# Kernel optimization log

Measured on AMD Instinct MI355X. Metric: run time of the kernel, lower is better.

## Reference

```python
import jax, jax.numpy as jnp
import numpy as np

B, S, D_IN, D_OUT = 4, 4096, 256, 256

def setup_inputs() -> dict:
    key = jax.random.key(0)
    ks = jax.random.split(key, 7)
    scale = 1.0 / np.sqrt(D_IN)
    return {
        "x": jax.random.normal(ks[0], (B, S, D_IN), dtype=jnp.float32),
        "Wq": jax.random.uniform(ks[1], (D_IN, D_OUT), jnp.float32, -scale, scale),
        "bq": jax.random.uniform(ks[2], (D_OUT,), jnp.float32, -scale, scale),
        "Wk": jax.random.uniform(ks[3], (D_IN, D_OUT), jnp.float32, -scale, scale),
        "bk": jax.random.uniform(ks[4], (D_OUT,), jnp.float32, -scale, scale),
        "Wv": jax.random.uniform(ks[5], (D_IN, D_OUT), jnp.float32, -scale, scale),
        "bv": jax.random.uniform(ks[6], (D_OUT,), jnp.float32, -scale, scale),
    }

def reference(x, Wq, bq, Wk, bk, Wv, bv):
    # QKV projections: [B, S, D_OUT]
    q = jnp.einsum("bsd,de->bse", x, Wq) + bq
    k = jnp.einsum("bsd,de->bse", x, Wk) + bk
    v = jnp.einsum("bsd,de->bse", x, Wv) + bv
    # Scaled dot-product attention; full [B, S, S] scores as in the original.
    scores = jnp.einsum("bqe,bke->bqk", q, k) / jnp.sqrt(jnp.asarray(q.shape[-1], q.dtype))
    attn = jax.nn.softmax(scores, axis=-1)
    return jnp.einsum("bqk,bke->bqe", attn, v)
```

## Files before the change

### kernel.cpp

```cpp
#include <hip/hip_runtime.h>
#include <stdint.h>

typedef unsigned short u16;
typedef long long i64;
typedef __attribute__((ext_vector_type(4))) float f32x4;
typedef __attribute__((ext_vector_type(8))) short bf16x8;
typedef __attribute__((ext_vector_type(4))) int i32x4;
typedef __attribute__((ext_vector_type(2))) unsigned int u32x2;

#define SEQ 4096
#define DIM 256
#define QS4 0.36067376f

__device__ __forceinline__ u16 f2bf(float f) {
  union { float f; uint32_t u; } v; v.f = f;
  uint32_t r = (v.u + 0x7FFFu + ((v.u >> 16) & 1u)) >> 16;
  return (u16)r;
}

__device__ __forceinline__ float bf2f(u16 u) {
  union { uint32_t u; float f; } v; v.u = ((uint32_t)u) << 16;
  return v.f;
}

__device__ __forceinline__ uint8_t f2fp8(float f) {
  return (uint8_t)__builtin_amdgcn_cvt_pk_fp8_f32(f, 0.f, 0, false);
}

__device__ __forceinline__ void gload_lds16(const void* g, void* lds) {
  __builtin_amdgcn_global_load_lds(
      (const __attribute__((address_space(1))) uint32_t*)g,
      (__attribute__((address_space(3))) uint32_t*)lds, 16, 0, 0);
}

__device__ __forceinline__ f32x4 mfma8(i64 a, i64 b, f32x4 c) {
  return __builtin_amdgcn_mfma_f32_16x16x32_fp8_fp8(a, b, c, 0, 0, 0);
}

__global__ __launch_bounds__(256) void wt_kernel(const float* __restrict__ Wq,
                                                 const float* __restrict__ Wk,
                                                 const float* __restrict__ Wv,
                                                 u16* __restrict__ wt) {
  int b = blockIdx.x;
  int w = b >> 8;
  int n = b & 255;
  const float* W = (w == 0) ? Wq : ((w == 1) ? Wk : Wv);
  float scale = (w == 0) ? QS4 : ((w == 1) ? 0.25f : 1.0f);
  int k = threadIdx.x;
  wt[(w * 256 + n) * 256 + k] = f2bf(W[k * 256 + n] * scale);
}

__global__ __launch_bounds__(256) void qkv_kernel(
    const float* __restrict__ x, const float* __restrict__ bq,
    const float* __restrict__ bk, const float* __restrict__ bv,
    const u16* __restrict__ wt, uint8_t* __restrict__ qs,
    uint8_t* __restrict__ kk, char* __restrict__ vt) {
  __shared__ __align__(16) char lds_b[65536];
  __shared__ __align__(16) u16 lds_v[4096];
  int tid = threadIdx.x;
  int w = tid >> 6, l = tid & 63;
  int a = l & 15, g = l >> 4;
  int rowbase = blockIdx.x * 64;

  uint32_t wso[8];
#pragma unroll
  for (int j = 0; j < 8; ++j) {
    uint32_t inst = w * 8 + j;
    uint32_t flat = inst * 1024 + l * 16;
    uint32_t row = flat >> 9;
    uint32_t c5 = (flat >> 4) & 31;
    uint32_t sc = (c5 & ~7u) | ((c5 ^ row) & 7u);
    wso[j] = row * 512 + sc * 16;
  }
  uint32_t bro[8];
#pragma unroll
  for (int ks = 0; ks < 8; ++ks) {
    uint32_t c5 = ks * 4 + g;
    uint32_t sc = (c5 & ~7u) | ((c5 ^ (a & 7u)) & 7u);
    bro[ks] = (uint32_t)a * 512 + sc * 16;
  }

  bf16x8 afr[8];
  {
    int row = rowbase + w * 16 + a;
    const f32x4* xr4 = (const f32x4*)(x + (size_t)row * 256);
#pragma unroll
    for (int ks = 0; ks < 8; ++ks) {
      int q4 = ks * 8 + g * 2;
      f32x4 lo = xr4[q4], hi = xr4[q4 + 1];
      union { bf16x8 s; u16 u[8]; } fr;
      fr.u[0] = f2bf(lo[0]); fr.u[1] = f2bf(lo[1]);
      fr.u[2] = f2bf(lo[2]); fr.u[3] = f2bf(lo[3]);
      fr.u[4] = f2bf(hi[0]); fr.u[5] = f2bf(hi[1]);
      fr.u[6] = f2bf(hi[2]); fr.u[7] = f2bf(hi[3]);
      afr[ks] = fr.s;
    }
  }

#pragma unroll
  for (int j = 0; j < 8; ++j)
    gload_lds16((const char*)wt + wso[j], lds_b + (w * 8 + j) * 1024);

  int cur = 0;
  for (int it = 0; it < 12; ++it) {
    asm volatile("s_waitcnt vmcnt(0) lgkmcnt(0)" ::: "memory");
    __builtin_amdgcn_s_barrier();
    __builtin_amdgcn_sched_barrier(0);
    if (it < 11) {
#pragma unroll
      for (int j = 0; j < 8; ++j)
        gload_lds16((const char*)wt + (size_t)(it + 1) * 32768 + wso[j],
                    lds_b + (cur ^ 1) * 32768 + (w * 8 + j) * 1024);
    }
    int w3 = it >> 2, qn = it & 3;
    f32x4 acc[4];
#pragma unroll
    for (int n0 = 0; n0 < 4; ++n0) acc[n0] = (f32x4){0.f, 0.f, 0.f, 0.f};
#pragma unroll
    for (int ks = 0; ks < 8; ++ks) {
#pragma unroll
      for (int n0 = 0; n0 < 4; ++n0) {
        bf16x8 bfr = *(const bf16x8*)(lds_b + cur * 32768 + bro[ks] + n0 * 8192);
        acc[n0] = __builtin_amdgcn_mfma_f32_16x16x32_bf16(afr[ks], bfr, acc[n0], 0, 0, 0);
      }
    }
    const float* bias = (w3 == 0) ? bq : ((w3 == 1) ? bk : bv);
    if (w3 < 2) {
      uint8_t* out8 = (w3 == 0) ? qs : kk;
      float bscale = (w3 == 0) ? QS4 : 0.25f;
#pragma unroll
      for (int n0 = 0; n0 < 4; ++n0) {
        int col = qn * 64 + n0 * 16 + a;
        float bb = bias[col] * bscale;
#pragma unroll
        for (int r = 0; r < 4; ++r) {
          int row = rowbase + w * 16 + g * 4 + r;
          out8[(size_t)row * 256 + col] = f2fp8(acc[n0][r] + bb);
        }
      }
    } else {
#pragma unroll
      for (int n0 = 0; n0 < 4; ++n0) {
        int col = qn * 64 + n0 * 16 + a;
        float bb = bias[col];
        int dl = n0 * 16 + a;
#pragma unroll
        for (int r = 0; r < 4; ++r) {
          int m = w * 16 + g * 4 + r;
          uint32_t byteoff =
              (uint32_t)dl * 128 + ((((uint32_t)m >> 3) ^ ((uint32_t)dl & 7)) << 4) + (m & 7) * 2;
          *(u16*)((char*)lds_v + byteoff) = f2bf(acc[n0][r] + bb);
        }
      }
      asm volatile("s_waitcnt lgkmcnt(0)" ::: "memory");
      __builtin_amdgcn_s_barrier();
      {
        int dl = tid >> 2;
        size_t base = (size_t)blockIdx.x * 32768 + (size_t)(qn * 64 + dl) * 128;
#pragma unroll
        for (int cc = 0; cc < 2; ++cc) {
          uint32_t c = (tid & 3) + cc * 4;
          i32x4 vd = *(const i32x4*)((const char*)lds_v + dl * 128 + ((c ^ (dl & 7)) << 4));
          *(i32x4*)(vt + base + c * 16) = vd;
        }
      }
    }
    cur ^= 1;
  }
}

#define VVB 32768u
#define PVB 98304u

#define PV_STEP(SLOT)                                                          \
  {                                                                            \
    bf16x8 pfr[2][2];                                                          \
    _Pragma("unroll") for (int mt = 0; mt < 2; ++mt)                           \
    _Pragma("unroll") for (int j2 = 0; j2 < 2; ++j2)                           \
        pfr[mt][j2] = *(const bf16x8*)(lds + PVB + (SLOT) * 16384 + pro[j2] +  \
                                       mt * 2048);                             \
    __builtin_amdgcn_s_setprio(1);                                             \
    _Pragma("unroll") for (int mt = 0; mt < 2; ++mt)                           \
    _Pragma("unroll") for (int j2 = 0; j2 < 2; ++j2)                           \
        lacc[mt] = __builtin_amdgcn_mfma_f32_16x16x32_bf16(pfr[mt][j2], ones,  \
                                                           lacc[mt], 0, 0, 0); \
    _Pragma("unroll") for (int d0 = 0; d0 < 8; ++d0)                           \
    _Pragma("unroll") for (int j2 = 0; j2 < 2; ++j2) {                         \
      bf16x8 vfr = *(const bf16x8*)(lds + VVB + (SLOT) * 32768 + vro[j2] +     \
                                    d0 * 2048);                                \
      o[0][d0] = __builtin_amdgcn_mfma_f32_16x16x32_bf16(pfr[0][j2], vfr, o[0][d0], 0, 0, 0); \
      o[1][d0] = __builtin_amdgcn_mfma_f32_16x16x32_bf16(pfr[1][j2], vfr, o[1][d0], 0, 0, 0); \
    }                                                                          \
    __builtin_amdgcn_s_setprio(0);                                             \
  }

#define QKEXP(CUR)                                                             \
  {                                                                            \
    f32x4 sc[2][2];                                                            \
    _Pragma("unroll") for (int mt = 0; mt < 2; ++mt)                           \
    _Pragma("unroll") for (int n = 0; n < 2; ++n)                              \
        sc[mt][n] = (f32x4){0.f, 0.f, 0.f, 0.f};                               \
    __builtin_amdgcn_s_setprio(1);                                             \
    _Pragma("unroll") for (int n = 0; n < 2; ++n)                              \
    _Pragma("unroll") for (int j = 0; j < 8; ++j) {                            \
      i64 kfr = *(const i64*)(lds + (CUR) * 16384 + kro[j] + n * 4096);        \
      sc[0][n] = mfma8(kfr, qfr[0][j], sc[0][n]);                              \
      sc[1][n] = mfma8(kfr, qfr[1][j], sc[1][n]);                              \
    }                                                                          \
    __builtin_amdgcn_s_setprio(0);                                             \
    _Pragma("unroll") for (int mt = 0; mt < 2; ++mt)                           \
    _Pragma("unroll") for (int n = 0; n < 2; ++n) {                            \
      float e0 = exp2f(sc[mt][n][0]);                                          \
      float e1 = exp2f(sc[mt][n][1]);                                          \
      float e2 = exp2f(sc[mt][n][2]);                                          \
      float e3 = exp2f(sc[mt][n][3]);                                          \
      uint32_t p0 = (uint32_t)f2bf(e0) | ((uint32_t)f2bf(e1) << 16);           \
      uint32_t p1 = (uint32_t)f2bf(e2) | ((uint32_t)f2bf(e3) << 16);           \
      u32x2 pk = {p0, p1};                                                     \
      *(u32x2*)(lds + PVB + (CUR) * 16384 + pwo[n] + mt * 2048) = pk;          \
    }                                                                          \
  }

#define TILE(CUR, DO_PV, DO_K)                                                 \
  {                                                                            \
    asm volatile("s_waitcnt vmcnt(0) lgkmcnt(0)" ::: "memory");                \
    __builtin_amdgcn_s_barrier();                                              \
    __builtin_amdgcn_sched_barrier(0);                                         \
    _Pragma("unroll") for (int j = 0; j < 4; ++j)                              \
        gload_lds16(vstp + vso[j], lds + VVB + (CUR) * 32768 + (w * 4 + j) * 1024); \
    if (DO_K) {                                                                \
      gload_lds16(kstp + kso[0], lds + ((CUR) ^ 1) * 16384 + (w * 2 + 0) * 1024); \
      gload_lds16(kstp + kso[1], lds + ((CUR) ^ 1) * 16384 + (w * 2 + 1) * 1024); \
    }                                                                          \
    kstp += 16384;                                                             \
    vstp += 32768;                                                             \
    if (w & 1) {                                                               \
      if (DO_PV) PV_STEP((CUR) ^ 1)                                            \
      QKEXP(CUR)                                                               \
    } else {                                                                   \
      QKEXP(CUR)                                                               \
      if (DO_PV) PV_STEP((CUR) ^ 1)                                            \
    }                                                                          \
  }

__global__ __launch_bounds__(512, 1) void attn_kernel(
    const uint8_t* __restrict__ qs, const uint8_t* __restrict__ kk,
    const char* __restrict__ vt, float* __restrict__ out,
    u16* __restrict__ pOB, float* __restrict__ pl, int split) {
  __shared__ __align__(16) char lds[131072];
  int tid = threadIdx.x;
  int w = tid >> 6, l = tid & 63;
  int a = l & 15, g = l >> 4;
  int qq = w >> 1, sub = w & 1;
  int bx = blockIdx.x;
  int h, batch, qt;
  if (split == 2) { h = bx & 1; batch = (bx >> 1) & 3; qt = bx >> 3; }
  else            { h = 0;      batch = (bx >> 1) & 3; qt = ((bx >> 3) << 1) | (bx & 1); }
  int ntHalf = (split == 2) ? 16 : 32;

  uint32_t a7 = a & 7;
  uint32_t kro[8], vro[2], pro[2], pwo[2], kso[2], vso[4];
  {
    uint32_t row = (uint32_t)(sub * 32 + a);
#pragma unroll
    for (int j = 0; j < 8; ++j) {
      uint32_t c4 = j * 2 + (g >> 1);
      kro[j] = row * 256 + (((c4 & ~7u) | ((c4 ^ a7) & 7u)) << 4) + (g & 1) * 8;
    }
  }
#pragma unroll
  for (int j2 = 0; j2 < 2; ++j2)
    vro[j2] = (uint32_t)(sub * 128 + a) * 128 +
              ((((uint32_t)(j2 * 4 + g)) ^ a7) << 4);
  {
    uint32_t q = (uint32_t)(qq * 32 + a);
#pragma unroll
    for (int j2 = 0; j2 < 2; ++j2)
      pro[j2] = q * 128 + ((((uint32_t)(j2 * 4 + g)) ^ a7) << 4);
#pragma unroll
    for (int n = 0; n < 2; ++n)
      pwo[n] = q * 128 +
               ((((uint32_t)(sub * 4 + n * 2 + (g >> 1))) ^ a7) << 4) + (g & 1) * 8;
  }
#pragma unroll
  for (int j = 0; j < 2; ++j) {
    uint32_t inst = w * 2 + j, flat = inst * 1024 + l * 16;
    uint32_t row = flat >> 8, c4 = (flat >> 4) & 15;
    kso[j] = row * 256 + (((c4 & ~7u) | ((c4 ^ (row & 7u)) & 7u)) << 4);
  }
#pragma unroll
  for (int j = 0; j < 4; ++j) {
    uint32_t inst = w * 4 + j, flat = inst * 1024 + l * 16;
    uint32_t row = flat >> 7, c3 = (flat >> 4) & 7;
    vso[j] = row * 128 + ((c3 ^ (row & 7)) << 4);
  }

  i64 qfr[2][8];
  {
    const uint8_t* qp = qs + (size_t)(batch * SEQ + qt * 128) * 256;
#pragma unroll
    for (int mt = 0; mt < 2; ++mt)
#pragma unroll
      for (int j = 0; j < 8; ++j)
        qfr[mt][j] = *(const i64*)(qp + (size_t)(qq * 32 + mt * 16 + a) * 256 +
                                   j * 32 + g * 8);
  }

  f32x4 o[2][8];
  f32x4 lacc[2];
#pragma unroll
  for (int mt = 0; mt < 2; ++mt) {
    lacc[mt] = (f32x4){0.f, 0.f, 0.f, 0.f};
#pragma unroll
    for (int d0 = 0; d0 < 8; ++d0) o[mt][d0] = (f32x4){0.f, 0.f, 0.f, 0.f};
  }
  const short ob = (short)0x3F80;
  bf16x8 ones = {ob, ob, ob, ob, ob, ob, ob, ob};

  const uint8_t* kstp = kk + (size_t)batch * SEQ * 256 + (size_t)h * 2048 * 256;
  const char* vstp = vt + (size_t)batch * 64 * 32768 + (size_t)h * 32 * 32768;

  gload_lds16(kstp + kso[0], lds + (w * 2 + 0) * 1024);
  gload_lds16(kstp + kso[1], lds + (w * 2 + 1) * 1024);
  kstp += 16384;

  TILE(0, false, true)
  for (int tp = 0; tp < ntHalf - 1; ++tp) {
    TILE(1, true, true)
    TILE(0, true, true)
  }
  TILE(1, true, false)

  asm volatile("s_waitcnt vmcnt(0) lgkmcnt(0)" ::: "memory");
  __builtin_amdgcn_s_barrier();
  __builtin_amdgcn_sched_barrier(0);
  PV_STEP(1)

  size_t obase = (size_t)(batch * SEQ + qt * 128 + qq * 32) * 256 + sub * 128;
  if (h == 0) {
#pragma unroll
    for (int mt = 0; mt < 2; ++mt)
#pragma unroll
      for (int r = 0; r < 4; ++r) {
#pragma unroll
        for (int d0 = 0; d0 < 8; ++d0)
          out[obase + (size_t)(mt * 16 + g * 4 + r) * 256 + d0 * 16 + a] = o[mt][d0][r];
      }
  } else {
#pragma unroll
    for (int mt = 0; mt < 2; ++mt)
#pragma unroll
      for (int r = 0; r < 4; ++r) {
#pragma unroll
        for (int d0 = 0; d0 < 8; ++d0)
          pOB[obase + (size_t)(mt * 16 + g * 4 + r) * 256 + d0 * 16 + a] =
              f2bf(o[mt][d0][r]);
      }
  }
  if (a == 0 && sub == 0) {
#pragma unroll
    for (int mt = 0; mt < 2; ++mt)
#pragma unroll
      for (int r = 0; r < 4; ++r)
        pl[h * 16384 + (batch * 32 + qt) * 128 + qq * 32 + mt * 16 + g * 4 + r] =
            lacc[mt][r];
  }
}

__global__ __launch_bounds__(256) void combine_kernel(float* __restrict__ out,
                                                      const u16* __restrict__ pOB,
                                                      const float* __restrict__ pl,
                                                      int split) {
  int b = blockIdx.x;
  int tid = threadIdx.x;
  int batch = b >> 12;
  int rem = b & 4095;
  int qt = rem >> 7, ql = rem & 127;
  size_t idx = (size_t)b * 256 + tid;
  int li = (batch * 32 + qt) * 128 + ql;
  float lA = pl[li];
  float v;
  if (split == 2) {
    float lB = pl[16384 + li];
    v = (out[idx] + bf2f(pOB[idx])) / (lA + lB);
  } else {
    v = out[idx] / lA;
  }
  out[idx] = v;
}

extern "C" void kernel_launch(void* const* d_in, const int* in_sizes, int n_in,
                              void* d_out, int out_size, void* d_ws, size_t ws_size,
                              hipStream_t stream) {
  const float* x = (const float*)d_in[0];
  const float* Wq = (const float*)d_in[1];
  const float* bq = (const float*)d_in[2];
  const float* Wk = (const float*)d_in[3];
  const float* bk = (const float*)d_in[4];
  const float* Wv = (const float*)d_in[5];
  const float* bv = (const float*)d_in[6];
  char* ws = (char*)d_ws;
  u16* wt = (u16*)ws;
  uint8_t* qs = (uint8_t*)(ws + 0x60000);
  uint8_t* kk = (uint8_t*)(ws + 0x460000);
  char* vt = ws + 0x860000;
  float* pl = (float*)(ws + 0x1060000);
  u16* pOB = (u16*)(ws + 0x1080000);
  int split = (ws_size >= 0x1880000ull) ? 2 : 1;
  wt_kernel<<<dim3(768), dim3(256), 0, stream>>>(Wq, Wk, Wv, wt);
  qkv_kernel<<<dim3(256), dim3(256), 0, stream>>>(x, bq, bk, bv, wt, qs, kk, vt);
  attn_kernel<<<dim3(split * 128), dim3(512), 0, stream>>>(qs, kk, vt, (float*)d_out,
                                                           pOB, pl, split);
  combine_kernel<<<dim3(16384), dim3(256), 0, stream>>>((float*)d_out, pOB, pl, split);
}
```

Baseline: 120.8 us.

## Split attention work across 16 waves per block instead of 8

Doubles the workgroup to 1024 threads, so each wave covers 16 key rows for QK and 64 output columns for PV instead of 32 and 128. This halves per-wave accumulator registers and per-wave work, aiming for more latency hiding through extra waves per CU. The alternating QK/PV ordering between wave pairs is dropped in favour of a fixed QK-then-PV order, and each wave issues fewer global-to-LDS loads. The cost is more waves contending at each barrier and a lost staggering of MFMA versus exp phases.

After: 114.1 us. -5.5%, faster.

```diff
diff --git a/kernel.cpp b/kernel.cpp
--- a/kernel.cpp
+++ b/kernel.cpp
@@ -184,7 +184,7 @@
     _Pragma("unroll") for (int j2 = 0; j2 < 2; ++j2)                           \
         lacc[mt] = __builtin_amdgcn_mfma_f32_16x16x32_bf16(pfr[mt][j2], ones,  \
                                                            lacc[mt], 0, 0, 0); \
-    _Pragma("unroll") for (int d0 = 0; d0 < 8; ++d0)                           \
+    _Pragma("unroll") for (int d0 = 0; d0 < 4; ++d0)                           \
     _Pragma("unroll") for (int j2 = 0; j2 < 2; ++j2) {                         \
       bf16x8 vfr = *(const bf16x8*)(lds + VVB + (SLOT) * 32768 + vro[j2] +     \
                                     d0 * 2048);                                \
@@ -194,56 +194,41 @@
     __builtin_amdgcn_s_setprio(0);                                             \
   }
 
-#define QKEXP(CUR)                                                             \
-  {                                                                            \
-    f32x4 sc[2][2];                                                            \
-    _Pragma("unroll") for (int mt = 0; mt < 2; ++mt)                           \
-    _Pragma("unroll") for (int n = 0; n < 2; ++n)                              \
-        sc[mt][n] = (f32x4){0.f, 0.f, 0.f, 0.f};                               \
-    __builtin_amdgcn_s_setprio(1);                                             \
-    _Pragma("unroll") for (int n = 0; n < 2; ++n)                              \
-    _Pragma("unroll") for (int j = 0; j < 8; ++j) {                            \
-      i64 kfr = *(const i64*)(lds + (CUR) * 16384 + kro[j] + n * 4096);        \
-      sc[0][n] = mfma8(kfr, qfr[0][j], sc[0][n]);                              \
-      sc[1][n] = mfma8(kfr, qfr[1][j], sc[1][n]);                              \
-    }                                                                          \
-    __builtin_amdgcn_s_setprio(0);                                             \
-    _Pragma("unroll") for (int mt = 0; mt < 2; ++mt)                           \
-    _Pragma("unroll") for (int n = 0; n < 2; ++n) {                            \
-      float e0 = exp2f(sc[mt][n][0]);                                          \
-      float e1 = exp2f(sc[mt][n][1]);                                          \
-      float e2 = exp2f(sc[mt][n][2]);                                          \
-      float e3 = exp2f(sc[mt][n][3]);                                          \
-      uint32_t p0 = (uint32_t)f2bf(e0) | ((uint32_t)f2bf(e1) << 16);           \
-      uint32_t p1 = (uint32_t)f2bf(e2) | ((uint32_t)f2bf(e3) << 16);           \
-      u32x2 pk = {p0, p1};                                                     \
-      *(u32x2*)(lds + PVB + (CUR) * 16384 + pwo[n] + mt * 2048) = pk;          \
-    }                                                                          \
-  }
-
 #define TILE(CUR, DO_PV, DO_K)                                                 \
   {                                                                            \
     asm volatile("s_waitcnt vmcnt(0) lgkmcnt(0)" ::: "memory");                \
     __builtin_amdgcn_s_barrier();                                              \
     __builtin_amdgcn_sched_barrier(0);                                         \
-    _Pragma("unroll") for (int j = 0; j < 4; ++j)                              \
-        gload_lds16(vstp + vso[j], lds + VVB + (CUR) * 32768 + (w * 4 + j) * 1024); \
-    if (DO_K) {                                                                \
-      gload_lds16(kstp + kso[0], lds + ((CUR) ^ 1) * 16384 + (w * 2 + 0) * 1024); \
-      gload_lds16(kstp + kso[1], lds + ((CUR) ^ 1) * 16384 + (w * 2 + 1) * 1024); \
-    }                                                                          \
+    gload_lds16(vstp + vso[0], lds + VVB + (CUR) * 32768 + (w * 2 + 0) * 1024); \
+    gload_lds16(vstp + vso[1], lds + VVB + (CUR) * 32768 + (w * 2 + 1) * 1024); \
+    if (DO_K)                                                                  \
+      gload_lds16(kstp + kso0, lds + ((CUR) ^ 1) * 16384 + w * 1024);          \
     kstp += 16384;                                                             \
     vstp += 32768;                                                             \
-    if (w & 1) {                                                               \
-      if (DO_PV) PV_STEP((CUR) ^ 1)                                            \
-      QKEXP(CUR)                                                               \
-    } else {                                                                   \
-      QKEXP(CUR)                                                               \
-      if (DO_PV) PV_STEP((CUR) ^ 1)                                            \
+    f32x4 sc[2];                                                               \
+    sc[0] = (f32x4){0.f, 0.f, 0.f, 0.f};                                       \
+    sc[1] = (f32x4){0.f, 0.f, 0.f, 0.f};                                       \
+    __builtin_amdgcn_s_setprio(1);                                             \
+    _Pragma("unroll") for (int j = 0; j < 8; ++j) {                            \
+      i64 kfr = *(const i64*)(lds + (CUR) * 16384 + kro[j]);                   \
+      sc[0] = mfma8(kfr, qfr[0][j], sc[0]);                                    \
+      sc[1] = mfma8(kfr, qfr[1][j], sc[1]);                                    \
     }                                                                          \
-  }
-
-__global__ __launch_bounds__(512, 1) void attn_kernel(
+    __builtin_amdgcn_s_setprio(0);                                             \
+    _Pragma("unroll") for (int mt = 0; mt < 2; ++mt) {                         \
+      float e0 = exp2f(sc[mt][0]);                                             \
+      float e1 = exp2f(sc[mt][1]);                                             \
+      float e2 = exp2f(sc[mt][2]);                                             \
+      float e3 = exp2f(sc[mt][3]);                                             \
+      uint32_t p0 = (uint32_t)f2bf(e0) | ((uint32_t)f2bf(e1) << 16);           \
+      uint32_t p1 = (uint32_t)f2bf(e2) | ((uint32_t)f2bf(e3) << 16);           \
+      u32x2 pk = {p0, p1};                                                     \
+      *(u32x2*)(lds + PVB + (CUR) * 16384 + pwo + mt * 2048) = pk;             \
+    }                                                                          \
+    if (DO_PV) PV_STEP((CUR) ^ 1)                                              \
+  }
+
+__global__ __launch_bounds__(1024, 1) void attn_kernel(
     const uint8_t* __restrict__ qs, const uint8_t* __restrict__ kk,
     const char* __restrict__ vt, float* __restrict__ out,
     u16* __restrict__ pOB, float* __restrict__ pl, int split) {
@@ -251,7 +236,7 @@
   int tid = threadIdx.x;
   int w = tid >> 6, l = tid & 63;
   int a = l & 15, g = l >> 4;
-  int qq = w >> 1, sub = w & 1;
+  int qq = w >> 2, sub = w & 3;
   int bx = blockIdx.x;
   int h, batch, qt;
   if (split == 2) { h = bx & 1; batch = (bx >> 1) & 3; qt = bx >> 3; }
@@ -259,9 +244,9 @@
   int ntHalf = (split == 2) ? 16 : 32;
 
   uint32_t a7 = a & 7;
-  uint32_t kro[8], vro[2], pro[2], pwo[2], kso[2], vso[4];
-  {
-    uint32_t row = (uint32_t)(sub * 32 + a);
+  uint32_t kro[8], vro[2], pro[2], pwo, kso0, vso[2];
+  {
+    uint32_t row = (uint32_t)(sub * 16 + a);
 #pragma unroll
     for (int j = 0; j < 8; ++j) {
       uint32_t c4 = j * 2 + (g >> 1);
@@ -270,27 +255,24 @@
   }
 #pragma unroll
   for (int j2 = 0; j2 < 2; ++j2)
-    vro[j2] = (uint32_t)(sub * 128 + a) * 128 +
+    vro[j2] = (uint32_t)(sub * 64 + a) * 128 +
               ((((uint32_t)(j2 * 4 + g)) ^ a7) << 4);
   {
     uint32_t q = (uint32_t)(qq * 32 + a);
 #pragma unroll
     for (int j2 = 0; j2 < 2; ++j2)
       pro[j2] = q * 128 + ((((uint32_t)(j2 * 4 + g)) ^ a7) << 4);
-#pragma unroll
-    for (int n = 0; n < 2; ++n)
-      pwo[n] = q * 128 +
-               ((((uint32_t)(sub * 4 + n * 2 + (g >> 1))) ^ a7) << 4) + (g & 1) * 8;
+    uint32_t tg = (uint32_t)(sub * 2 + (g >> 1));
+    pwo = q * 128 + ((tg ^ a7) << 4) + (g & 1) * 8;
+  }
+  {
+    uint32_t flat = (uint32_t)w * 1024 + l * 16;
+    uint32_t row = flat >> 8, c4 = (flat >> 4) & 15;
+    kso0 = row * 256 + (((c4 & ~7u) | ((c4 ^ (row & 7u)) & 7u)) << 4);
   }
 #pragma unroll
   for (int j = 0; j < 2; ++j) {
     uint32_t inst = w * 2 + j, flat = inst * 1024 + l * 16;
-    uint32_t row = flat >> 8, c4 = (flat >> 4) & 15;
-    kso[j] = row * 256 + (((c4 & ~7u) | ((c4 ^ (row & 7u)) & 7u)) << 4);
-  }
-#pragma unroll
-  for (int j = 0; j < 4; ++j) {
-    uint32_t inst = w * 4 + j, flat = inst * 1024 + l * 16;
     uint32_t row = flat >> 7, c3 = (flat >> 4) & 7;
     vso[j] = row * 128 + ((c3 ^ (row & 7)) << 4);
   }
@@ -306,13 +288,13 @@
                                    j * 32 + g * 8);
   }
 
-  f32x4 o[2][8];
+  f32x4 o[2][4];
   f32x4 lacc[2];
 #pragma unroll
   for (int mt = 0; mt < 2; ++mt) {
     lacc[mt] = (f32x4){0.f, 0.f, 0.f, 0.f};
 #pragma unroll
-    for (int d0 = 0; d0 < 8; ++d0) o[mt][d0] = (f32x4){0.f, 0.f, 0.f, 0.f};
+    for (int d0 = 0; d0 < 4; ++d0) o[mt][d0] = (f32x4){0.f, 0.f, 0.f, 0.f};
   }
   const short ob = (short)0x3F80;
   bf16x8 ones = {ob, ob, ob, ob, ob, ob, ob, ob};
@@ -320,8 +302,7 @@
   const uint8_t* kstp = kk + (size_t)batch * SEQ * 256 + (size_t)h * 2048 * 256;
   const char* vstp = vt + (size_t)batch * 64 * 32768 + (size_t)h * 32 * 32768;
 
-  gload_lds16(kstp + kso[0], lds + (w * 2 + 0) * 1024);
-  gload_lds16(kstp + kso[1], lds + (w * 2 + 1) * 1024);
+  gload_lds16(kstp + kso0, lds + w * 1024);
   kstp += 16384;
 
   TILE(0, false, true)
@@ -336,14 +317,14 @@
   __builtin_amdgcn_sched_barrier(0);
   PV_STEP(1)
 
-  size_t obase = (size_t)(batch * SEQ + qt * 128 + qq * 32) * 256 + sub * 128;
+  size_t obase = (size_t)(batch * SEQ + qt * 128 + qq * 32) * 256 + sub * 64;
   if (h == 0) {
 #pragma unroll
     for (int mt = 0; mt < 2; ++mt)
 #pragma unroll
       for (int r = 0; r < 4; ++r) {
 #pragma unroll
-        for (int d0 = 0; d0 < 8; ++d0)
+        for (int d0 = 0; d0 < 4; ++d0)
           out[obase + (size_t)(mt * 16 + g * 4 + r) * 256 + d0 * 16 + a] = o[mt][d0][r];
       }
   } else {
@@ -352,7 +333,7 @@
 #pragma unroll
       for (int r = 0; r < 4; ++r) {
 #pragma unroll
-        for (int d0 = 0; d0 < 8; ++d0)
+        for (int d0 = 0; d0 < 4; ++d0)
           pOB[obase + (size_t)(mt * 16 + g * 4 + r) * 256 + d0 * 16 + a] =
               f2bf(o[mt][d0][r]);
       }
@@ -409,7 +390,7 @@
   int split = (ws_size >= 0x1880000ull) ? 2 : 1;
   wt_kernel<<<dim3(768), dim3(256), 0, stream>>>(Wq, Wk, Wv, wt);
   qkv_kernel<<<dim3(256), dim3(256), 0, stream>>>(x, bq, bk, bv, wt, qs, kk, vt);
-  attn_kernel<<<dim3(split * 128), dim3(512), 0, stream>>>(qs, kk, vt, (float*)d_out,
-                                                           pOB, pl, split);
+  attn_kernel<<<dim3(split * 128), dim3(1024), 0, stream>>>(qs, kk, vt, (float*)d_out,
+                                                            pOB, pl, split);
   combine_kernel<<<dim3(16384), dim3(256), 0, stream>>>((float*)d_out, pOB, pl, split);
 }
```
